# Kernel optimization log

Hardware: AMD Instinct MI355X
Metric: run time of the kernel (lower is better)

The kernel has to match this reference:

```python
import jax, jax.numpy as jnp
import numpy as np

B, T, C, H, HD = 2, 2048, 768, 12, 64


def setup_inputs() -> dict:
    key = jax.random.key(0)
    k0, k1, k2, k3 = jax.random.split(key, 4)
    x = jax.random.normal(k0, (B, T, C), dtype=jnp.float32)
    w_attn = jax.random.normal(k1, (3 * H * HD, C), dtype=jnp.float32) * 0.02
    b_attn = jnp.zeros((3 * H * HD,), dtype=jnp.float32)
    w_proj = jax.random.normal(k2, (C, H * HD), dtype=jnp.float32) * 0.02
    b_proj = jnp.zeros((C,), dtype=jnp.float32)
    sel_w = jax.random.normal(k3, (H,), dtype=jnp.float32) * 0.3
    return {"x": x, "w_attn": w_attn, "b_attn": b_attn,
            "w_proj": w_proj, "b_proj": b_proj, "sel_w": sel_w}


def reference(x, w_attn, b_attn, w_proj, b_proj, sel_w):
    Bc, Tc, Cc = x.shape
    Hc = sel_w.shape[0]
    HDc = w_attn.shape[0] // (3 * Hc)
    qkv = x @ w_attn.T + b_attn                          # [B,T,3*H*HD]
    q, k, v = jnp.split(qkv, 3, axis=2)
    q = q.reshape(Bc, Tc, Hc, HDc).transpose(0, 2, 1, 3)  # [B,H,T,HD]
    k = k.reshape(Bc, Tc, Hc, HDc).transpose(0, 2, 1, 3)
    v = v.reshape(Bc, Tc, Hc, HDc).transpose(0, 2, 1, 3)

    scale = 1.0 / np.sqrt(HDc).astype(np.float32)
    att = jnp.einsum('bhid,bhjd->bhij', q, k) * scale    # [B,H,T,T]
    causal = jnp.tril(jnp.ones((Tc, Tc), dtype=bool))
    neg_inf = jnp.asarray(-jnp.inf, dtype=att.dtype)
    att = jnp.where(causal[None, None], att, neg_inf)

    # selection head: per-head linear combo of (causally-zeroed) logits
    att0 = jnp.where(causal[None, None], att, 0.0)       # -inf -> 0 before combo
    S = jnp.einsum('bhij,h->bij', att0, sel_w)           # [B,T,T], bias=False
    S = jnp.where(causal[None], S, 0.0)
    S = jax.nn.relu(S)
    S = S.at[..., 0].set(0.0)                            # protect_bos_token
    S = S * (1.0 - jnp.eye(Tc, dtype=S.dtype))           # prevent_from_masking_myself

    FF = jnp.cumsum(S, axis=-2)                          # forgetting accumulation over rows
    FF_shifted = jnp.concatenate(
        [jnp.zeros_like(FF[..., :1, :]), FF[..., :-1, :]], axis=-2)

    att = jax.nn.softmax(att - FF_shifted[:, None], axis=-1)
    y = jnp.einsum('bhij,bhjd->bhid', att, v)            # [B,H,T,HD]
    y = y.transpose(0, 2, 1, 3).reshape(Bc, Tc, Hc * HDc)
    return y @ w_proj.T + b_proj
```

## Files before the change

### kernel.cpp

```cpp
#include <hip/hip_runtime.h>

#define B_   2
#define T_   2048
#define C_   768
#define H_   12
#define HD_  64
#define M_   (B_ * T_)
#define N3_  (3 * C_)
#define KB_  (C_ * 2)

typedef __bf16 bf16_t;
typedef bf16_t bf16x8 __attribute__((ext_vector_type(8)));
typedef float  floatx4 __attribute__((ext_vector_type(4)));
typedef unsigned long long u64_t;

__device__ inline floatx4 mfma_bf16(bf16x8 a, bf16x8 b, floatx4 c) {
    return __builtin_amdgcn_mfma_f32_16x16x32_bf16(a, b, c, 0, 0, 0);
}

__device__ __forceinline__ void async_copy16(const void* g, void* l) {
    __builtin_amdgcn_global_load_lds(
        (const __attribute__((address_space(1))) void*)g,
        (__attribute__((address_space(3))) void*)l, 16, 0, 0);
}

__device__ __forceinline__ bf16x8 frag_read(const char* ldsbase, int row, int quad) {
    int slot = quad ^ ((row >> 1) & 3);
    return *(const bf16x8*)(ldsbase + row * 64 + slot * 16);
}

template<bool TRIPLE>
__device__ __forceinline__ void gemm_loop8(
    const char* Ah, const char* Al, const char* Bh, const char* Bl,
    char* lds, floatx4 (&acc)[4][2])
{
    int tid = threadIdx.x, lane = tid & 63, wave = tid >> 6;
    int l15 = lane & 15, quad = lane >> 4;
    int wr = wave >> 2, wc = wave & 3;
    const int PH = TRIPLE ? 32768 : 16384;
    auto stage1 = [&](const char* tile, char* base, int k0) {
        int p = tid;
        int r = p >> 2, slot = p & 3;
        int g = slot ^ ((r >> 1) & 3);
        async_copy16(tile + (size_t)r * KB_ + k0 + g * 16, base + p * 16);
    };
    auto stage = [&](int ph, int k0) {
        char* base = lds + ph * PH;
        stage1(Ah, base, k0);
        stage1(Bh, base + 8192, k0);
        if (TRIPLE) {
            stage1(Al, base + 16384, k0);
            stage1(Bl, base + 24576, k0);
        }
    };
    stage(0, 0);
    int ph = 0;
#pragma unroll 1
    for (int k0 = 0; k0 < KB_; k0 += 64) {
        __syncthreads();
        if (k0 + 64 < KB_) stage(ph ^ 1, k0 + 64);
        char* base = lds + ph * PH;
        bf16x8 ah[4], al[4], bh[2], bl[2];
#pragma unroll
        for (int t = 0; t < 4; ++t) {
            ah[t] = frag_read(base, wr * 64 + t * 16 + l15, quad);
            if (TRIPLE)
                al[t] = frag_read(base + 16384, wr * 64 + t * 16 + l15, quad);
        }
#pragma unroll
        for (int t = 0; t < 2; ++t) {
            bh[t] = frag_read(base + 8192, wc * 32 + t * 16 + l15, quad);
            if (TRIPLE)
                bl[t] = frag_read(base + 24576, wc * 32 + t * 16 + l15, quad);
        }
#pragma unroll
        for (int mi = 0; mi < 4; ++mi)
#pragma unroll
            for (int ni = 0; ni < 2; ++ni) {
                acc[mi][ni] = mfma_bf16(ah[mi], bh[ni], acc[mi][ni]);
                if (TRIPLE) {
                    acc[mi][ni] = mfma_bf16(ah[mi], bl[ni], acc[mi][ni]);
                    acc[mi][ni] = mfma_bf16(al[mi], bh[ni], acc[mi][ni]);
                }
            }
        ph ^= 1;
    }
}

__global__ __launch_bounds__(256) void prep_kernel(
    const float* __restrict__ x, const float* __restrict__ w_attn,
    const float* __restrict__ w_proj,
    bf16_t* __restrict__ x_hi, bf16_t* __restrict__ x_lo,
    bf16_t* __restrict__ w_hi, bf16_t* __restrict__ w_lo,
    bf16_t* __restrict__ wp_b, int nx4, int nw4, int np4)
{
    int g4 = blockIdx.x * 256 + threadIdx.x;
    union U { bf16_t e[4]; u64_t v; };
    if (g4 < nx4) {
        float4 f = ((const float4*)x)[g4];
        U h, l;
        h.e[0] = (bf16_t)f.x; l.e[0] = (bf16_t)(f.x - (float)h.e[0]);
        h.e[1] = (bf16_t)f.y; l.e[1] = (bf16_t)(f.y - (float)h.e[1]);
        h.e[2] = (bf16_t)f.z; l.e[2] = (bf16_t)(f.z - (float)h.e[2]);
        h.e[3] = (bf16_t)f.w; l.e[3] = (bf16_t)(f.w - (float)h.e[3]);
        ((u64_t*)x_hi)[g4] = h.v;
        ((u64_t*)x_lo)[g4] = l.v;
    } else if (g4 < nx4 + nw4) {
        int i = g4 - nx4;
        float4 f = ((const float4*)w_attn)[i];
        U h, l;
        h.e[0] = (bf16_t)f.x; l.e[0] = (bf16_t)(f.x - (float)h.e[0]);
        h.e[1] = (bf16_t)f.y; l.e[1] = (bf16_t)(f.y - (float)h.e[1]);
        h.e[2] = (bf16_t)f.z; l.e[2] = (bf16_t)(f.z - (float)h.e[2]);
        h.e[3] = (bf16_t)f.w; l.e[3] = (bf16_t)(f.w - (float)h.e[3]);
        ((u64_t*)w_hi)[i] = h.v;
        ((u64_t*)w_lo)[i] = l.v;
    } else if (g4 < nx4 + nw4 + np4) {
        int i = g4 - nx4 - nw4;
        float4 f = ((const float4*)w_proj)[i];
        U h;
        h.e[0] = (bf16_t)f.x;
        h.e[1] = (bf16_t)f.y;
        h.e[2] = (bf16_t)f.z;
        h.e[3] = (bf16_t)f.w;
        ((u64_t*)wp_b)[i] = h.v;
    }
}

__global__ __launch_bounds__(512) void qkv_gemm(
    const bf16_t* __restrict__ x_hi, const bf16_t* __restrict__ x_lo,
    const bf16_t* __restrict__ w_hi, const bf16_t* __restrict__ w_lo,
    const float* __restrict__ bias, const float* __restrict__ selw,
    bf16_t* __restrict__ q_hi, bf16_t* __restrict__ q_lo,
    bf16_t* __restrict__ kw_hi, bf16_t* __restrict__ kw_lo,
    bf16_t* __restrict__ k_b, bf16_t* __restrict__ vt)
{
    extern __shared__ char lds[];
    int m0 = blockIdx.x * 128, n0 = blockIdx.y * 128;
    floatx4 acc[4][2];
#pragma unroll
    for (int i = 0; i < 4; ++i)
#pragma unroll
        for (int j = 0; j < 2; ++j) acc[i][j] = (floatx4){0.f, 0.f, 0.f, 0.f};
    if (n0 >= 2 * C_) {
        gemm_loop8<false>((const char*)(x_hi + (size_t)m0 * C_), nullptr,
                          (const char*)(w_hi + (size_t)n0 * C_), nullptr, lds, acc);
    } else {
        gemm_loop8<true>((const char*)(x_hi + (size_t)m0 * C_),
                         (const char*)(x_lo + (size_t)m0 * C_),
                         (const char*)(w_hi + (size_t)n0 * C_),
                         (const char*)(w_lo + (size_t)n0 * C_), lds, acc);
    }

    int tid = threadIdx.x, lane = tid & 63, wave = tid >> 6;
    int l15 = lane & 15, quad = lane >> 4;
    int wr = wave >> 2, wc = wave & 3;

    if (n0 >= 2 * C_) {
        __syncthreads();
        bf16_t* TL = (bf16_t*)lds;
#pragma unroll
        for (int ni = 0; ni < 2; ++ni) {
            int colp = wc * 32 + ni * 16 + l15;
            float bb = bias[n0 + colp];
#pragma unroll
            for (int mi = 0; mi < 4; ++mi)
#pragma unroll
                for (int r = 0; r < 4; ++r) {
                    int rowp = wr * 64 + mi * 16 + quad * 4 + r;
                    TL[colp * 136 + rowp] = (bf16_t)(acc[mi][ni][r] + bb);
                }
        }
        __syncthreads();
        int colp = tid >> 2, sub = tid & 3;
        int cg = n0 - 2 * C_ + colp;
        int h  = cg >> 6, hd = cg & 63;
        int bb = m0 >> 11;
        int t0 = m0 - bb * T_;
        bf16_t* dst = vt + (((size_t)(bb * H_ + h) * HD_ + hd) * T_) + t0 + sub * 32;
        const bf16_t* srcl = TL + colp * 136 + sub * 32;
#pragma unroll
        for (int k = 0; k < 4; ++k)
            *(int4*)(dst + k * 8) = *(const int4*)(srcl + k * 8);
        return;
    }

    int cb = n0 + wc * 32;
#pragma unroll
    for (int ni = 0; ni < 2; ++ni) {
        int col = cb + ni * 16 + l15;
        float bb = bias[col];
#pragma unroll
        for (int mi = 0; mi < 4; ++mi)
#pragma unroll
            for (int r = 0; r < 4; ++r) {
                int row = m0 + wr * 64 + mi * 16 + quad * 4 + r;
                float v = acc[mi][ni][r] + bb;
                if (cb < C_) {
                    float vs = v * 0.125f;
                    bf16_t h = (bf16_t)vs;
                    q_hi[(size_t)row * C_ + col] = h;
                    q_lo[(size_t)row * C_ + col] = (bf16_t)(vs - (float)h);
                } else {
                    int c2 = col - C_;
                    k_b[(size_t)row * C_ + c2] = (bf16_t)v;
                    float kw = v * selw[c2 >> 6];
                    bf16_t h = (bf16_t)kw;
                    kw_hi[(size_t)row * C_ + c2] = h;
                    kw_lo[(size_t)row * C_ + c2] = (bf16_t)(kw - (float)h);
                }
            }
    }
}

#define SEG_    16
#define SEGLEN_ (T_ / SEG_)

__global__ __launch_bounds__(512) void s_gemm(
    const bf16_t* __restrict__ q_hi, const bf16_t* __restrict__ q_lo,
    const bf16_t* __restrict__ kw_hi, const bf16_t* __restrict__ kw_lo,
    float* __restrict__ SF, float* __restrict__ segsum)
{
    extern __shared__ char lds[];
    int t = blockIdx.x, b = blockIdx.z;
    int it = (int)((sqrtf(8.f * t + 1.f) - 1.f) * 0.5f);
    while ((it + 1) * (it + 2) / 2 <= t) ++it;
    while (it * (it + 1) / 2 > t) --it;
    int jt = t - it * (it + 1) / 2;
    int i0 = it * 128, j0 = jt * 128;
    float* out = SF + (size_t)b * T_ * T_;

    floatx4 acc[4][2];
#pragma unroll
    for (int i = 0; i < 4; ++i)
#pragma unroll
        for (int j = 0; j < 2; ++j) acc[i][j] = (floatx4){0.f, 0.f, 0.f, 0.f};
    size_t arow = ((size_t)b * T_ + i0) * C_;
    size_t brow = ((size_t)b * T_ + j0) * C_;
    gemm_loop8<true>((const char*)(q_hi + arow), (const char*)(q_lo + arow),
                     (const char*)(kw_hi + brow), (const char*)(kw_lo + brow),
                     lds, acc);

    int tid = threadIdx.x, lane = tid & 63, wave = tid >> 6;
    int l15 = lane & 15, quad = lane >> 4;
    int wr = wave >> 2, wc = wave & 3;
    float colsum[2] = {0.f, 0.f};
#pragma unroll
    for (int ni = 0; ni < 2; ++ni) {
        int j = j0 + wc * 32 + ni * 16 + l15;
#pragma unroll
        for (int mi = 0; mi < 4; ++mi)
#pragma unroll
            for (int r = 0; r < 4; ++r) {
                int i = i0 + wr * 64 + mi * 16 + quad * 4 + r;
                float s = acc[mi][ni][r];
                s = (j >= 1 && j < i) ? fmaxf(s, 0.f) : 0.f;
                out[(size_t)i * T_ + j] = s;
                colsum[ni] += s;
            }
    }
#pragma unroll
    for (int ni = 0; ni < 2; ++ni) {
        colsum[ni] += __shfl_xor(colsum[ni], 16);
        colsum[ni] += __shfl_xor(colsum[ni], 32);
    }
    float* red = (float*)lds;
    if (quad == 0) {
#pragma unroll
        for (int ni = 0; ni < 2; ++ni)
            red[wr * 128 + wc * 32 + ni * 16 + l15] = colsum[ni];
    }
    __syncthreads();
    if (tid < 128) {
        float ssum = red[tid] + red[128 + tid];
        segsum[((size_t)b * SEG_ + it) * T_ + j0 + tid] = ssum;
    }
}

__global__ __launch_bounds__(256) void scan_apply(
    float* __restrict__ SF, const float* __restrict__ segsum)
{
    int gid  = blockIdx.x * 256 + threadIdx.x;
    int j    = gid & (T_ - 1);
    int rest = gid >> 11;
    int seg  = rest & (SEG_ - 1);
    int b    = rest >> 4;
    if (seg * SEGLEN_ + SEGLEN_ - 1 < j) return;
    float run = 0.f;
    for (int s = 0; s < seg; ++s) {
        float v = (s * SEGLEN_ + SEGLEN_ - 1 <= j) ? 0.f
                : segsum[((size_t)b * SEG_ + s) * T_ + j];
        run += v;
    }
    float* col = SF + (size_t)b * T_ * T_ + (size_t)(seg * SEGLEN_) * T_ + j;
#pragma unroll 4
    for (int i = 0; i < SEGLEN_; ++i) {
        float s = col[(size_t)i * T_];
        s = (seg * SEGLEN_ + i > j) ? s : 0.f;
        col[(size_t)i * T_] = run;
        run += s;
    }
}

__global__ __launch_bounds__(256) void attn_kernel(
    const bf16_t* __restrict__ q_b, const bf16_t* __restrict__ k_b,
    const bf16_t* __restrict__ vt_g, const float* __restrict__ FF,
    bf16_t* __restrict__ y_b, float* __restrict__ opart,
    float* __restrict__ lpart)
{
    extern __shared__ __align__(16) char lds[];
    char* KL = lds;
    char* VL = lds + 32768;
    bf16_t* PBall = (bf16_t*)(lds + 65536);

    int tid = threadIdx.x, lane = tid & 63, wave = tid >> 6;
    int l15 = lane & 15, quad = lane >> 4;
    int u = blockIdx.x & 15, g = blockIdx.x >> 4;
    int tile, jlo, jhi, half;
    bool split;
    if (g == 0)      { tile = 16 + u; jlo = 0; jhi = 7;                   half = 0; split = true;  }
    else if (g == 1) { tile = u;      jlo = 0; jhi = ((u + 2) >> 1) - 1;  half = 0; split = false; }
    else             { tile = 31 - u; jlo = 8; jhi = ((33 - u) >> 1) - 1; half = 1; split = true;  }
    int h = blockIdx.y, b = blockIdx.z;
    int i0w = tile * 64 + wave * 16;
    const floatx4 fzero = {0.f, 0.f, 0.f, 0.f};

    const bf16_t* qrow = q_b + ((size_t)b * T_ + i0w + l15) * C_ + h * HD_;
    bf16x8 qa0 = *(const bf16x8*)(qrow + quad * 8);
    bf16x8 qa1 = *(const bf16x8*)(qrow + 32 + quad * 8);

    const bf16_t* kbase = k_b + (size_t)b * T_ * C_ + h * HD_;
    const bf16_t* vbase = vt_g + (size_t)(b * H_ + h) * HD_ * T_;
    const float* fpr[4];
#pragma unroll
    for (int r = 0; r < 4; ++r)
        fpr[r] = FF + ((size_t)b * T_ + i0w + quad * 4 + r) * T_ + jlo * 128 + l15;

    auto stage = [&](int ph, int j0) {
#pragma unroll
        for (int i = 0; i < 4; ++i) {
            int p = (wave * 4 + i) * 64 + lane;
            int r = p >> 3, sp = p & 7, s = sp ^ (r & 7);
            async_copy16(kbase + (size_t)(j0 + r) * C_ + s * 8,
                         KL + ph * 16384 + p * 16);
        }
#pragma unroll
        for (int i = 0; i < 4; ++i) {
            int p = (wave * 4 + i) * 64 + lane;
            int r = p >> 4, sp = p & 15;
            int s = (sp & 8) | ((sp & 7) ^ (r & 7));
            async_copy16(vbase + (size_t)r * T_ + j0 + s * 8,
                         VL + ph * 16384 + p * 16);
        }
    };

    float l_lane[4] = {0.f, 0.f, 0.f, 0.f};
    floatx4 O[4];
#pragma unroll
    for (int nt = 0; nt < 4; ++nt) O[nt] = fzero;

    stage(0, jlo * 128);
    int ph = 0;
#pragma unroll 1
    for (int jc = jlo; jc <= jhi; ++jc) {
        __syncthreads();
        if (jc < jhi) stage(ph ^ 1, (jc + 1) * 128);

        float ff[8][4];
#pragma unroll
        for (int r = 0; r < 4; ++r) {
#pragma unroll
            for (int s = 0; s < 8; ++s) ff[s][r] = fpr[r][s * 16];
            fpr[r] += 128;
        }
        const char* KLp = KL + ph * 16384;
        floatx4 pc[8];
#pragma unroll
        for (int s = 0; s < 8; ++s) {
            int r = s * 16 + l15;
            bf16x8 k0 = *(const bf16x8*)&KLp[r * 128 + ((quad     ^ (r & 7)) * 16)];
            bf16x8 k1 = *(const bf16x8*)&KLp[r * 128 + (((quad+4) ^ (r & 7)) * 16)];
            floatx4 p = mfma_bf16(qa0, k0, fzero);
            pc[s] = mfma_bf16(qa1, k1, p);
        }
        bool diag = (jc * 128 + 127 > i0w);
        float p[8][4];
#pragma unroll
        for (int s = 0; s < 8; ++s)
#pragma unroll
            for (int r = 0; r < 4; ++r) {
                float lg = pc[s][r] - ff[s][r] - 20.f;
                if (diag) {
                    int i = i0w + quad * 4 + r;
                    int j = jc * 128 + s * 16 + l15;
                    lg = (j <= i) ? lg : -__builtin_inff();
                }
                p[s][r] = __expf(lg);
            }
#pragma unroll
        for (int r = 0; r < 4; ++r)
            l_lane[r] += ((p[0][r] + p[1][r]) + (p[2][r] + p[3][r]))
                       + ((p[4][r] + p[5][r]) + (p[6][r] + p[7][r]));

        bf16_t* Pw = PBall + wave * 2048;
#pragma unroll
        for (int s = 0; s < 8; ++s)
#pragma unroll
            for (int r = 0; r < 4; ++r) {
                int rr = quad * 4 + r;
                int c  = s * 2 + (l15 >> 3);
                int ch = (c & 8) | ((c & 7) ^ (rr & 7));
                Pw[rr * 128 + ch * 8 + (l15 & 7)] = (bf16_t)p[s][r];
            }
        asm volatile("s_waitcnt lgkmcnt(0)" ::: "memory");
        int xk = l15 & 7;
        bf16x8 pa[4];
#pragma unroll
        for (int gk = 0; gk < 4; ++gk) {
            int c  = gk * 4 + quad;
            int ch = (c & 8) | ((c & 7) ^ xk);
            pa[gk] = *(const bf16x8*)&Pw[l15 * 128 + ch * 8];
        }
        const char* VLp = VL + ph * 16384;
#pragma unroll
        for (int nt = 0; nt < 4; ++nt) {
            int rv = nt * 16 + l15;
#pragma unroll
            for (int gk = 0; gk < 4; ++gk) {
                int c  = gk * 4 + quad;
                int ch = (c & 8) | ((c & 7) ^ (rv & 7));
                bf16x8 v = *(const bf16x8*)&VLp[rv * 256 + ch * 16];
                O[nt] = mfma_bf16(pa[gk], v, O[nt]);
            }
        }
        ph ^= 1;
    }

#pragma unroll
    for (int r = 0; r < 4; ++r)
#pragma unroll
        for (int d = 1; d < 16; d <<= 1)
            l_lane[r] += __shfl_xor(l_lane[r], d);

    if (!split) {
#pragma unroll
        for (int r = 0; r < 4; ++r) {
            float inv = 1.f / l_lane[r];
            int i = i0w + quad * 4 + r;
#pragma unroll
            for (int nt = 0; nt < 4; ++nt)
                y_b[((size_t)b * T_ + i) * C_ + h * HD_ + nt * 16 + l15] =
                    (bf16_t)(O[nt][r] * inv);
        }
    } else {
        size_t ob = ((((size_t)(b * H_ + h) * 16 + (tile - 16)) * 2 + half) * 4096);
#pragma unroll
        for (int r = 0; r < 4; ++r) {
            int rl = wave * 16 + quad * 4 + r;
#pragma unroll
            for (int nt = 0; nt < 4; ++nt)
                opart[ob + (size_t)rl * 64 + nt * 16 + l15] = O[nt][r];
        }
        if (l15 == 0) {
            size_t lb = (((size_t)(b * H_ + h) * 16 + (tile - 16)) * 2 + half) * 64;
#pragma unroll
            for (int r = 0; r < 4; ++r)
                lpart[lb + wave * 16 + quad * 4 + r] = l_lane[r];
        }
    }
}

__global__ __launch_bounds__(256) void merge_kernel(
    const float* __restrict__ opart, const float* __restrict__ lpart,
    bf16_t* __restrict__ y_b)
{
    int tt = blockIdx.x, h = blockIdx.y, b = blockIdx.z;
    size_t b0 = (((size_t)(b * H_ + h) * 16 + tt) * 2) * 4096;
    size_t l0 = (((size_t)(b * H_ + h) * 16 + tt) * 2) * 64;
    int tile = 16 + tt;
#pragma unroll 4
    for (int e = threadIdx.x; e < 4096; e += 256) {
        int row = e >> 6, col = e & 63;
        float l = lpart[l0 + row] + lpart[l0 + 64 + row];
        float o = opart[b0 + e] + opart[b0 + 4096 + e];
        y_b[((size_t)b * T_ + tile * 64 + row) * C_ + h * HD_ + col] =
            (bf16_t)(o / l);
    }
}

__global__ __launch_bounds__(512) void proj_gemm(
    const bf16_t* __restrict__ y_b, const bf16_t* __restrict__ wp_b,
    const float* __restrict__ bias, float* __restrict__ out)
{
    extern __shared__ char lds[];
    int m0 = blockIdx.x * 128, n0 = blockIdx.y * 128;
    floatx4 acc[4][2];
#pragma unroll
    for (int i = 0; i < 4; ++i)
#pragma unroll
        for (int j = 0; j < 2; ++j) acc[i][j] = (floatx4){0.f, 0.f, 0.f, 0.f};
    gemm_loop8<false>((const char*)(y_b + (size_t)m0 * C_), nullptr,
                      (const char*)(wp_b + (size_t)n0 * C_), nullptr, lds, acc);

    int tid = threadIdx.x, lane = tid & 63, wave = tid >> 6;
    int l15 = lane & 15, quad = lane >> 4;
    int wr = wave >> 2, wc = wave & 3;
#pragma unroll
    for (int ni = 0; ni < 2; ++ni) {
        int col = n0 + wc * 32 + ni * 16 + l15;
        float bb = bias[col];
#pragma unroll
        for (int mi = 0; mi < 4; ++mi)
#pragma unroll
            for (int r = 0; r < 4; ++r)
                out[(size_t)(m0 + wr * 64 + mi * 16 + quad * 4 + r) * C_ + col] =
                    acc[mi][ni][r] + bb;
    }
}

extern "C" void kernel_launch(void* const* d_in, const int* in_sizes, int n_in,
                              void* d_out, int out_size, void* d_ws, size_t ws_size,
                              hipStream_t stream)
{
    const float* x      = (const float*)d_in[0];
    const float* w_attn = (const float*)d_in[1];
    const float* b_attn = (const float*)d_in[2];
    const float* w_proj = (const float*)d_in[3];
    const float* b_proj = (const float*)d_in[4];
    const float* sel_w  = (const float*)d_in[5];
    float* out = (float*)d_out;

    char* ws = (char*)d_ws;
    size_t off = 0;
    auto alloc = [&](size_t bytes) {
        void* p = ws + off;
        off += (bytes + 255) & ~(size_t)255;
        return p;
    };
    const size_t MC2 = (size_t)M_ * C_ * 2;
    bf16_t* q_hi   = (bf16_t*)alloc(MC2);
    bf16_t* kw_hi  = (bf16_t*)alloc(MC2);
    bf16_t* k_b    = (bf16_t*)alloc(MC2);
    bf16_t* y_b    = (bf16_t*)alloc(MC2);
    bf16_t* wp_b   = (bf16_t*)alloc((size_t)C_ * C_ * 2);
    float*  segsum = (float*)alloc((size_t)B_ * SEG_ * T_ * 4);
    float*  lpart  = (float*)alloc((size_t)B_ * H_ * 16 * 2 * 64 * 4);
    char* dead_base = (char*)alloc(3 * MC2);
    bf16_t* q_lo  = (bf16_t*)dead_base;
    bf16_t* kw_lo = (bf16_t*)(dead_base + MC2);
    bf16_t* vt    = (bf16_t*)(dead_base + 2 * MC2);
    float*  opart = (float*)dead_base;
    char* shared_base = (char*)alloc((size_t)B_ * T_ * T_ * 4);
    bf16_t* x_hi = (bf16_t*)shared_base;
    bf16_t* x_lo = (bf16_t*)(shared_base + MC2);
    bf16_t* w_hi = (bf16_t*)(shared_base + 2 * MC2);
    bf16_t* w_lo = (bf16_t*)(shared_base + 2 * MC2 + (size_t)N3_ * C_ * 2);
    float*  SF   = (float*)shared_base;

    int nx = M_ * C_, nw = N3_ * C_, np = C_ * C_;
    int ntot4 = (nx + nw + np) / 4;
    prep_kernel<<<dim3((ntot4 + 255) / 256), 256, 0, stream>>>(
        x, w_attn, w_proj, x_hi, x_lo, w_hi, w_lo, wp_b, nx / 4, nw / 4, np / 4);

    qkv_gemm<<<dim3(M_ / 128, N3_ / 128), 512, 65536, stream>>>(
        x_hi, x_lo, w_hi, w_lo, b_attn, sel_w,
        q_hi, q_lo, kw_hi, kw_lo, k_b, vt);
    s_gemm<<<dim3(136, 1, B_), 512, 65536, stream>>>(
        q_hi, q_lo, kw_hi, kw_lo, SF, segsum);
    scan_apply<<<dim3(B_ * SEG_ * T_ / 256), 256, 0, stream>>>(SF, segsum);
    attn_kernel<<<dim3(48, H_, B_), 256, 81920, stream>>>(
        q_hi, k_b, vt, SF, y_b, opart, lpart);
    merge_kernel<<<dim3(16, H_, B_), 256, 0, stream>>>(opart, lpart, y_b);
    proj_gemm<<<dim3(M_ / 128, C_ / 128), 512, 32768, stream>>>(y_b, wp_b, b_proj, out);
}
```

Before: 248.9 us.

## Process two heads per attention block to share FF loads, halve key chunk

Each attention block now handles two heads (h and h+6) with the same query rows, so the per-row FF forgetting matrix loaded from global memory is reused across both heads instead of being read once per head. The key chunk size drops from 128 to 64 columns, and LDS moves from dynamic to static allocation at a smaller total size. The grid halves in the head dimension, which reduces block count and parallelism. Register pressure also rises from holding two sets of accumulators, which may hurt occupancy.

```diff
diff --git a/kernel.cpp b/kernel.cpp
--- a/kernel.cpp
+++ b/kernel.cpp
@@ -308,166 +308,163 @@
     bf16_t* __restrict__ y_b, float* __restrict__ opart,
     float* __restrict__ lpart)
 {
-    extern __shared__ __align__(16) char lds[];
-    char* KL = lds;
-    char* VL = lds + 32768;
-    bf16_t* PBall = (bf16_t*)(lds + 65536);
+    __shared__ __align__(16) char KL[2][2][8192];
+    __shared__ __align__(16) char VL[2][2][8192];
+    __shared__ __align__(16) bf16_t PB[4][1024];
 
     int tid = threadIdx.x, lane = tid & 63, wave = tid >> 6;
     int l15 = lane & 15, quad = lane >> 4;
     int u = blockIdx.x & 15, g = blockIdx.x >> 4;
     int tile, jlo, jhi, half;
     bool split;
-    if (g == 0)      { tile = 16 + u; jlo = 0; jhi = 7;                   half = 0; split = true;  }
-    else if (g == 1) { tile = u;      jlo = 0; jhi = ((u + 2) >> 1) - 1;  half = 0; split = false; }
-    else             { tile = 31 - u; jlo = 8; jhi = ((33 - u) >> 1) - 1; half = 1; split = true;  }
-    int h = blockIdx.y, b = blockIdx.z;
+    if (g == 0)      { tile = 16 + u; jlo = 0;  jhi = 15;       half = 0; split = true;  }
+    else if (g == 1) { tile = u;      jlo = 0;  jhi = u;        half = 0; split = false; }
+    else             { tile = 31 - u; jlo = 16; jhi = 31 - u;   half = 1; split = true;  }
+    int h0 = blockIdx.y, h1 = blockIdx.y + 6, b = blockIdx.z;
     int i0w = tile * 64 + wave * 16;
     const floatx4 fzero = {0.f, 0.f, 0.f, 0.f};
 
-    const bf16_t* qrow = q_b + ((size_t)b * T_ + i0w + l15) * C_ + h * HD_;
-    bf16x8 qa0 = *(const bf16x8*)(qrow + quad * 8);
-    bf16x8 qa1 = *(const bf16x8*)(qrow + 32 + quad * 8);
-
-    const bf16_t* kbase = k_b + (size_t)b * T_ * C_ + h * HD_;
-    const bf16_t* vbase = vt_g + (size_t)(b * H_ + h) * HD_ * T_;
+    const bf16_t* qr0 = q_b + ((size_t)b * T_ + i0w + l15) * C_ + h0 * HD_;
+    const bf16_t* qr1 = q_b + ((size_t)b * T_ + i0w + l15) * C_ + h1 * HD_;
+    bf16x8 qa0_0 = *(const bf16x8*)(qr0 + quad * 8);
+    bf16x8 qa1_0 = *(const bf16x8*)(qr0 + 32 + quad * 8);
+    bf16x8 qa0_1 = *(const bf16x8*)(qr1 + quad * 8);
+    bf16x8 qa1_1 = *(const bf16x8*)(qr1 + 32 + quad * 8);
+
+    const bf16_t* kb0 = k_b + (size_t)b * T_ * C_ + h0 * HD_;
+    const bf16_t* kb1 = k_b + (size_t)b * T_ * C_ + h1 * HD_;
+    const bf16_t* vb0 = vt_g + (size_t)(b * H_ + h0) * HD_ * T_;
+    const bf16_t* vb1 = vt_g + (size_t)(b * H_ + h1) * HD_ * T_;
+
     const float* fpr[4];
 #pragma unroll
     for (int r = 0; r < 4; ++r)
-        fpr[r] = FF + ((size_t)b * T_ + i0w + quad * 4 + r) * T_ + jlo * 128 + l15;
+        fpr[r] = FF + ((size_t)b * T_ + i0w + quad * 4 + r) * T_ + jlo * 64 + l15;
 
     auto stage = [&](int ph, int j0) {
 #pragma unroll
-        for (int i = 0; i < 4; ++i) {
-            int p = (wave * 4 + i) * 64 + lane;
+        for (int i = 0; i < 2; ++i) {
+            int p = (wave * 2 + i) * 64 + lane;
             int r = p >> 3, sp = p & 7, s = sp ^ (r & 7);
-            async_copy16(kbase + (size_t)(j0 + r) * C_ + s * 8,
-                         KL + ph * 16384 + p * 16);
-        }
-#pragma unroll
-        for (int i = 0; i < 4; ++i) {
-            int p = (wave * 4 + i) * 64 + lane;
-            int r = p >> 4, sp = p & 15;
-            int s = (sp & 8) | ((sp & 7) ^ (r & 7));
-            async_copy16(vbase + (size_t)r * T_ + j0 + s * 8,
-                         VL + ph * 16384 + p * 16);
+            async_copy16(kb0 + (size_t)(j0 + r) * C_ + s * 8, &KL[ph][0][p * 16]);
+            async_copy16(kb1 + (size_t)(j0 + r) * C_ + s * 8, &KL[ph][1][p * 16]);
+            async_copy16(vb0 + (size_t)r * T_ + j0 + s * 8, &VL[ph][0][p * 16]);
+            async_copy16(vb1 + (size_t)r * T_ + j0 + s * 8, &VL[ph][1][p * 16]);
         }
     };
 
-    float l_lane[4] = {0.f, 0.f, 0.f, 0.f};
-    floatx4 O[4];
-#pragma unroll
-    for (int nt = 0; nt < 4; ++nt) O[nt] = fzero;
-
-    stage(0, jlo * 128);
+    float l0[4] = {0.f, 0.f, 0.f, 0.f}, l1[4] = {0.f, 0.f, 0.f, 0.f};
+    floatx4 O0[4], O1[4];
+#pragma unroll
+    for (int nt = 0; nt < 4; ++nt) { O0[nt] = fzero; O1[nt] = fzero; }
+
+    stage(0, jlo * 64);
     int ph = 0;
 #pragma unroll 1
     for (int jc = jlo; jc <= jhi; ++jc) {
         __syncthreads();
-        if (jc < jhi) stage(ph ^ 1, (jc + 1) * 128);
-
-        float ff[8][4];
+        if (jc < jhi) stage(ph ^ 1, (jc + 1) * 64);
+
+        float ff[4][4];
 #pragma unroll
         for (int r = 0; r < 4; ++r) {
 #pragma unroll
-            for (int s = 0; s < 8; ++s) ff[s][r] = fpr[r][s * 16];
-            fpr[r] += 128;
-        }
-        const char* KLp = KL + ph * 16384;
-        floatx4 pc[8];
-#pragma unroll
-        for (int s = 0; s < 8; ++s) {
-            int r = s * 16 + l15;
-            bf16x8 k0 = *(const bf16x8*)&KLp[r * 128 + ((quad     ^ (r & 7)) * 16)];
-            bf16x8 k1 = *(const bf16x8*)&KLp[r * 128 + (((quad+4) ^ (r & 7)) * 16)];
-            floatx4 p = mfma_bf16(qa0, k0, fzero);
-            pc[s] = mfma_bf16(qa1, k1, p);
-        }
-        bool diag = (jc * 128 + 127 > i0w);
-        float p[8][4];
-#pragma unroll
-        for (int s = 0; s < 8; ++s)
+            for (int s = 0; s < 4; ++s) ff[s][r] = fpr[r][s * 16];
+            fpr[r] += 64;
+        }
+        bool diag = (jc * 64 + 63 > i0w);
+
+        auto do_head = [&](const char* KLh, const char* VLh,
+                           bf16x8 qa0, bf16x8 qa1,
+                           floatx4 (&O)[4], float (&l_lane)[4]) {
+            floatx4 pc[4];
+#pragma unroll
+            for (int s = 0; s < 4; ++s) {
+                int r = s * 16 + l15;
+                bf16x8 k0 = *(const bf16x8*)&KLh[r * 128 + ((quad     ^ (r & 7)) * 16)];
+                bf16x8 k1 = *(const bf16x8*)&KLh[r * 128 + (((quad+4) ^ (r & 7)) * 16)];
+                floatx4 p = mfma_bf16(qa0, k0, fzero);
+                pc[s] = mfma_bf16(qa1, k1, p);
+            }
+            float p[4][4];
+#pragma unroll
+            for (int s = 0; s < 4; ++s)
+#pragma unroll
+                for (int r = 0; r < 4; ++r) {
+                    float lg = pc[s][r] - ff[s][r] - 20.f;
+                    if (diag) {
+                        int i = i0w + quad * 4 + r;
+                        int j = jc * 64 + s * 16 + l15;
+                        lg = (j <= i) ? lg : -__builtin_inff();
+                    }
+                    p[s][r] = __expf(lg);
+                }
+#pragma unroll
+            for (int r = 0; r < 4; ++r)
+                l_lane[r] += (p[0][r] + p[1][r]) + (p[2][r] + p[3][r]);
+
+            bf16_t* Pw = PB[wave];
+#pragma unroll
+            for (int s = 0; s < 4; ++s)
+#pragma unroll
+                for (int r = 0; r < 4; ++r) {
+                    int rr = quad * 4 + r;
+                    int ch = (s * 2 + (l15 >> 3)) ^ (rr & 7);
+                    Pw[rr * 64 + ch * 8 + (l15 & 7)] = (bf16_t)p[s][r];
+                }
+            asm volatile("s_waitcnt lgkmcnt(0)" ::: "memory");
+            int xk = l15 & 7;
+            bf16x8 pa0 = *(const bf16x8*)&Pw[l15 * 64 + ((quad ^ xk) * 8)];
+            bf16x8 pa1 = *(const bf16x8*)&Pw[l15 * 64 + (((4 + quad) ^ xk) * 8)];
+#pragma unroll
+            for (int nt = 0; nt < 4; ++nt) {
+                int rv = nt * 16 + l15;
+                bf16x8 v0 = *(const bf16x8*)&VLh[rv * 128 + ((quad     ^ (rv & 7)) * 16)];
+                bf16x8 v1 = *(const bf16x8*)&VLh[rv * 128 + (((quad+4) ^ (rv & 7)) * 16)];
+                O[nt] = mfma_bf16(pa0, v0, O[nt]);
+                O[nt] = mfma_bf16(pa1, v1, O[nt]);
+            }
+        };
+        do_head(&KL[ph][0][0], &VL[ph][0][0], qa0_0, qa1_0, O0, l0);
+        do_head(&KL[ph][1][0], &VL[ph][1][0], qa0_1, qa1_1, O1, l1);
+        ph ^= 1;
+    }
+
+    auto fin = [&](floatx4 (&O)[4], float (&l_lane)[4], int h) {
+#pragma unroll
+        for (int r = 0; r < 4; ++r)
+#pragma unroll
+            for (int d = 1; d < 16; d <<= 1)
+                l_lane[r] += __shfl_xor(l_lane[r], d);
+        if (!split) {
 #pragma unroll
             for (int r = 0; r < 4; ++r) {
-                float lg = pc[s][r] - ff[s][r] - 20.f;
-                if (diag) {
-                    int i = i0w + quad * 4 + r;
-                    int j = jc * 128 + s * 16 + l15;
-                    lg = (j <= i) ? lg : -__builtin_inff();
-                }
-                p[s][r] = __expf(lg);
-            }
-#pragma unroll
-        for (int r = 0; r < 4; ++r)
-            l_lane[r] += ((p[0][r] + p[1][r]) + (p[2][r] + p[3][r]))
-                       + ((p[4][r] + p[5][r]) + (p[6][r] + p[7][r]));
-
-        bf16_t* Pw = PBall + wave * 2048;
-#pragma unroll
-        for (int s = 0; s < 8; ++s)
+                float inv = 1.f / l_lane[r];
+                int i = i0w + quad * 4 + r;
+#pragma unroll
+                for (int nt = 0; nt < 4; ++nt)
+                    y_b[((size_t)b * T_ + i) * C_ + h * HD_ + nt * 16 + l15] =
+                        (bf16_t)(O[nt][r] * inv);
+            }
+        } else {
+            size_t ob = ((((size_t)(b * H_ + h) * 16 + (tile - 16)) * 2 + half) * 4096);
 #pragma unroll
             for (int r = 0; r < 4; ++r) {
-                int rr = quad * 4 + r;
-                int c  = s * 2 + (l15 >> 3);
-                int ch = (c & 8) | ((c & 7) ^ (rr & 7));
-                Pw[rr * 128 + ch * 8 + (l15 & 7)] = (bf16_t)p[s][r];
-            }
-        asm volatile("s_waitcnt lgkmcnt(0)" ::: "memory");
-        int xk = l15 & 7;
-        bf16x8 pa[4];
-#pragma unroll
-        for (int gk = 0; gk < 4; ++gk) {
-            int c  = gk * 4 + quad;
-            int ch = (c & 8) | ((c & 7) ^ xk);
-            pa[gk] = *(const bf16x8*)&Pw[l15 * 128 + ch * 8];
-        }
-        const char* VLp = VL + ph * 16384;
-#pragma unroll
-        for (int nt = 0; nt < 4; ++nt) {
-            int rv = nt * 16 + l15;
-#pragma unroll
-            for (int gk = 0; gk < 4; ++gk) {
-                int c  = gk * 4 + quad;
-                int ch = (c & 8) | ((c & 7) ^ (rv & 7));
-                bf16x8 v = *(const bf16x8*)&VLp[rv * 256 + ch * 16];
-                O[nt] = mfma_bf16(pa[gk], v, O[nt]);
-            }
-        }
-        ph ^= 1;
-    }
-
-#pragma unroll
-    for (int r = 0; r < 4; ++r)
-#pragma unroll
-        for (int d = 1; d < 16; d <<= 1)
-            l_lane[r] += __shfl_xor(l_lane[r], d);
-
-    if (!split) {
-#pragma unroll
-        for (int r = 0; r < 4; ++r) {
-            float inv = 1.f / l_lane[r];
-            int i = i0w + quad * 4 + r;
-#pragma unroll
-            for (int nt = 0; nt < 4; ++nt)
-                y_b[((size_t)b * T_ + i) * C_ + h * HD_ + nt * 16 + l15] =
-                    (bf16_t)(O[nt][r] * inv);
-        }
-    } else {
-        size_t ob = ((((size_t)(b * H_ + h) * 16 + (tile - 16)) * 2 + half) * 4096);
-#pragma unroll
-        for (int r = 0; r < 4; ++r) {
-            int rl = wave * 16 + quad * 4 + r;
-#pragma unroll
-            for (int nt = 0; nt < 4; ++nt)
-                opart[ob + (size_t)rl * 64 + nt * 16 + l15] = O[nt][r];
-        }
-        if (l15 == 0) {
-            size_t lb = (((size_t)(b * H_ + h) * 16 + (tile - 16)) * 2 + half) * 64;
-#pragma unroll
-            for (int r = 0; r < 4; ++r)
-                lpart[lb + wave * 16 + quad * 4 + r] = l_lane[r];
-        }
-    }
+                int rl = wave * 16 + quad * 4 + r;
+#pragma unroll
+                for (int nt = 0; nt < 4; ++nt)
+                    opart[ob + (size_t)rl * 64 + nt * 16 + l15] = O[nt][r];
+            }
+            if (l15 == 0) {
+                size_t lb = (((size_t)(b * H_ + h) * 16 + (tile - 16)) * 2 + half) * 64;
+#pragma unroll
+                for (int r = 0; r < 4; ++r)
+                    lpart[lb + wave * 16 + quad * 4 + r] = l_lane[r];
+            }
+        }
+    };
+    fin(O0, l0, h0);
+    fin(O1, l1, h1);
 }
 
 __global__ __launch_bounds__(256) void merge_kernel(
@@ -568,7 +565,7 @@
     s_gemm<<<dim3(136, 1, B_), 512, 65536, stream>>>(
         q_hi, q_lo, kw_hi, kw_lo, SF, segsum);
     scan_apply<<<dim3(B_ * SEG_ * T_ / 256), 256, 0, stream>>>(SF, segsum);
-    attn_kernel<<<dim3(48, H_, B_), 256, 81920, stream>>>(
+    attn_kernel<<<dim3(48, 6, B_), 256, 0, stream>>>(
         q_hi, k_b, vt, SF, y_b, opart, lpart);
     merge_kernel<<<dim3(16, H_, B_), 256, 0, stream>>>(opart, lpart, y_b);
     proj_gemm<<<dim3(M_ / 128, C_ / 128), 512, 32768, stream>>>(y_b, wp_b, b_proj, out);
```

Measured after the change: 260.9 us. +4.8%, slower.
